# Kernel tuning notes

Measured on AMD Instinct MI355X. Metric: run time of the kernel, lower is better.

## Reference

```python
import jax, jax.numpy as jnp
import numpy as np

B, H, N, D = 2, 16, 4096, 64
NUM_PROJS = 8
BLOCK_SIZE = 256
SAMPLE_SIZE = 256
SCALE = D ** -0.5  # default scale = dim ** -0.5


def _unit_hamming_distance_array(size_n):
    # Gray-code permutation so that adjacent hash buckets differ in one bit
    a = np.array([0, 1], dtype=np.int32)
    for _ in range(size_n - 1):
        a = np.concatenate([a, np.flip(a) + a.shape[0]])
    return a

_PERM = jnp.asarray(_unit_hamming_distance_array(NUM_PROJS))
_ENC = jnp.asarray(2 ** np.arange(NUM_PROJS, dtype=np.int32))  # [num_projs]


def lsh_hash(x, proj_dir):
    # x: [b,h,n,d], proj_dir: [d,r] -> bucket id per token: [b,h,n]
    proj = jnp.einsum('bhnd,dr->bhnr', x, proj_dir)
    bin_ids = jnp.sum((proj > 0).astype(jnp.int32) * _ENC, axis=-1)
    return _PERM[bin_ids]


def attn_lse(q, k, v, scale):
    # exact softmax attention returning output and log-sum-exp
    s = jnp.einsum('...md,...nd->...mn', q, k) * scale
    lse = jax.nn.logsumexp(s, axis=-1, keepdims=True)
    out = jnp.einsum('...mn,...nv->...mv', jnp.exp(s - lse), v)
    return out, lse


def gather_seq(x, idx):
    # gather along the sequence axis (axis=2); broadcasts over last dim
    return jnp.take_along_axis(x, idx[..., None], axis=2)


def add_self_attentions(attn1, lse1, attn2, lse2):
    # combine two un-normalized softmax attentions via their lse's
    c = jax.nn.sigmoid(lse1 - lse2)  # = 1/(1+exp(lse2-lse1))
    attn = c * attn1 + (1.0 - c) * attn2
    lse = jnp.logaddexp(lse1, lse2)
    return attn, lse


def setup_inputs() -> dict:
    key = jax.random.key(0)
    kq, kk, kv, kp, ks = jax.random.split(key, 5)
    return {
        'query': jax.random.normal(kq, (B, H, N, D), jnp.float32),
        'key': jax.random.normal(kk, (B, H, N, D), jnp.float32),
        'value': jax.random.normal(kv, (B, H, N, D), jnp.float32),
        'proj_dir': jax.random.normal(kp, (D, NUM_PROJS), jnp.float32),
        'sampled_set': jax.random.randint(ks, (B, H, SAMPLE_SIZE), 0, N, dtype=jnp.int32),
    }


def reference(query, key, value, proj_dir, sampled_set):
    # --- LSH bucketing + stable sort of queries/keys by bucket id ---
    q_idx = jnp.argsort(lsh_hash(query, proj_dir), axis=2, stable=True)
    k_idx = jnp.argsort(lsh_hash(key, proj_dir), axis=2, stable=True)
    q_idx_inv = jnp.argsort(q_idx, axis=2, stable=True)

    q_s = gather_seq(query, q_idx)
    k_s = gather_seq(key, k_idx)
    v_s = gather_seq(value, k_idx)

    # --- block-diagonal attention in sorted order ---
    nb = N // BLOCK_SIZE
    q_b = q_s.reshape(B, H, nb, BLOCK_SIZE, D)
    k_b = k_s.reshape(B, H, nb, BLOCK_SIZE, D)
    v_b = v_s.reshape(B, H, nb, BLOCK_SIZE, D)
    attn_blk, lse_blk = attn_lse(q_b, k_b, v_b, SCALE)
    attn_blk = attn_blk.reshape(B, H, N, D)
    lse_blk = lse_blk.reshape(B, H, N, 1)
    # un-sort back to original query order
    attn_blk = gather_seq(attn_blk, q_idx_inv)
    lse_blk = gather_seq(lse_blk, q_idx_inv)

    # --- uniformly sampled residual attention, importance-weighted ---
    k_sub = gather_seq(key, sampled_set)
    v_sub = gather_seq(value, sampled_set)
    attn_res, lse_res = attn_lse(query, k_sub, v_sub, SCALE)
    lse_res = lse_res + jnp.log(N / SAMPLE_SIZE)

    attn, lse = add_self_attentions(attn_blk, lse_blk, attn_res, lse_res)
    return attn
```

## Files before the change

### kernel.cpp

```cpp
#include <hip/hip_runtime.h>
#include <hip/hip_bf16.h>
#include <math.h>

#define BH_ 32
#define N_ 4096
#define D_ 64
#define SAMP_ 256
#define SCALE_ 0.125f
#define LOG16_ 2.7725887222397811f
#define HPAD 68

typedef __attribute__((ext_vector_type(4))) float f32x4;
typedef __attribute__((ext_vector_type(8))) short bf16x8;
typedef __attribute__((ext_vector_type(4))) short bf16x4;

static __device__ __forceinline__ unsigned pack2(float a, float b) {
    union { __hip_bfloat162 h; unsigned u; } c;
    c.h = __float22bfloat162_rn(make_float2(a, b));
    return c.u;
}

static __device__ __forceinline__ bf16x8 cvt8v(f32x4 a, f32x4 b) {
    union { unsigned u[4]; bf16x8 v; } r;
    r.u[0] = pack2(a[0], a[1]); r.u[1] = pack2(a[2], a[3]);
    r.u[2] = pack2(b[0], b[1]); r.u[3] = pack2(b[2], b[3]);
    return r.v;
}

static __device__ __forceinline__ bf16x8 cvt8(const float* p) {
    return cvt8v(*(const f32x4*)p, *(const f32x4*)(p + 4));
}

__global__ __launch_bounds__(128) void hash_kernel(
    const float* __restrict__ q, const float* __restrict__ k,
    const float* __restrict__ pd,
    unsigned char* __restrict__ qbuck, unsigned char* __restrict__ kbuck)
{
    extern __shared__ char smraw[];
    float*  Xs  = (float*)smraw;
    double* Pdl = (double*)(smraw + 128 * HPAD * 4);

    int tid = threadIdx.x;
    const float* src = blockIdx.y ? k : q;
    unsigned char* dst = blockIdx.y ? kbuck : qbuck;
    size_t tok0 = (size_t)blockIdx.x * 128;

    {
        int d = tid >> 1, r0 = (tid & 1) * 4;
#pragma unroll
        for (int j = 0; j < 4; ++j)
            Pdl[d * 8 + r0 + j] = (double)pd[d * 8 + r0 + j];
    }
    {
        const float4* src4 = (const float4*)(src + tok0 * D_);
        for (int i = tid; i < 128 * 16; i += 128) {
            int r = i >> 4, c = i & 15;
            *(float4*)&Xs[r * HPAD + c * 4] = src4[i];
        }
    }
    __syncthreads();

    float xr[64];
#pragma unroll
    for (int c = 0; c < 16; ++c)
        *(f32x4*)&xr[c * 4] = *(const f32x4*)&Xs[tid * HPAD + c * 4];

    double acc[8];
#pragma unroll
    for (int r = 0; r < 8; ++r) acc[r] = 0.0;
#pragma unroll
    for (int d = 0; d < 64; ++d) {
        double x = (double)xr[d];
        const double* pr = Pdl + d * 8;
#pragma unroll
        for (int r = 0; r < 8; ++r) acc[r] += x * pr[r];
    }
    int bin = 0;
#pragma unroll
    for (int r = 0; r < 8; ++r)
        if (acc[r] > 0.0) bin |= (1 << r);
    dst[tok0 + tid] = (unsigned char)(bin ^ (bin >> 1));
}

__global__ __launch_bounds__(256) void sort_kernel(
    const unsigned char* __restrict__ qbuck,
    const unsigned char* __restrict__ kbuck,
    int* __restrict__ q_idx, int* __restrict__ k_idx)
{
    __shared__ unsigned short hist[64][256];
    __shared__ unsigned int   binstart[256];
    __shared__ alignas(16) unsigned char bl[N_];

    int bh = blockIdx.x, tensor = blockIdx.y;
    const unsigned char* buck = (tensor ? kbuck : qbuck) + bh * N_;
    int* idx_out = (tensor ? k_idx : q_idx) + bh * N_;
    int t = threadIdx.x;

    ((uint4*)bl)[t] = ((const uint4*)buck)[t];
    {
        uint4* h4 = (uint4*)&hist[0][0];
        for (int i = t; i < 2048; i += 256) h4[i] = make_uint4(0, 0, 0, 0);
    }
    __syncthreads();

    if (t < 64) {
        for (int u = 0; u < 64; ++u) hist[t][bl[t * 64 + u]]++;
    }
    __syncthreads();

    {
        unsigned run = 0;
        for (int tt = 0; tt < 64; ++tt) {
            unsigned c = hist[tt][t];
            hist[tt][t] = (unsigned short)run;
            run += c;
        }
        binstart[t] = run;
    }
    __syncthreads();

    if (t < 64) {
        unsigned b0 = binstart[t*4], b1 = binstart[t*4+1],
                 b2 = binstart[t*4+2], b3 = binstart[t*4+3];
        unsigned s = b0 + b1 + b2 + b3, p = s;
#pragma unroll
        for (int d = 1; d < 64; d <<= 1) {
            unsigned y = __shfl_up(p, d);
            if (t >= d) p += y;
        }
        unsigned e = p - s;
        binstart[t*4]   = e;
        binstart[t*4+1] = e + b0;
        binstart[t*4+2] = e + b0 + b1;
        binstart[t*4+3] = e + b0 + b1 + b2;
    }
    __syncthreads();

    if (t < 64) {
        for (int u = 0; u < 64; ++u) {
            int tok = t * 64 + u;
            int b = bl[tok];
            int pos = (int)(binstart[b] + hist[t][b]);
            hist[t][b]++;
            idx_out[pos] = tok;
        }
    }
}

static __device__ __forceinline__ void stage_kv(
    const float* __restrict__ key, const float* __restrict__ value,
    size_t base, int krI, int v0, int v1, int v2, int v3,
    int hK, int kwofs, int vd, int tid, short* Ksm, short* Vsm)
{
    {
        const float* kp = key + (base + (size_t)krI) * D_ + hK * 32;
        f32x4 k0 = *(const f32x4*)kp,        k1 = *(const f32x4*)(kp + 4);
        f32x4 k2 = *(const f32x4*)(kp + 8),  k3 = *(const f32x4*)(kp + 12);
        f32x4 k4 = *(const f32x4*)(kp + 16), k5 = *(const f32x4*)(kp + 20);
        f32x4 k6 = *(const f32x4*)(kp + 24), k7 = *(const f32x4*)(kp + 28);
        *(bf16x8*)&Ksm[kwofs]       = cvt8v(k0, k1);
        *(bf16x8*)&Ksm[kwofs + 128] = cvt8v(k2, k3);
        *(bf16x8*)&Ksm[kwofs + 256] = cvt8v(k4, k5);
        *(bf16x8*)&Ksm[kwofs + 384] = cvt8v(k6, k7);
    }
    {
        const float* vp0 = value + (base + (size_t)v0) * D_ + vd;
        const float* vp1 = value + (base + (size_t)v1) * D_ + vd;
        const float* vp2 = value + (base + (size_t)v2) * D_ + vd;
        const float* vp3 = value + (base + (size_t)v3) * D_ + vd;
        f32x4 a0 = *(const f32x4*)vp0, b0 = *(const f32x4*)(vp0 + 4);
        f32x4 a1 = *(const f32x4*)vp1, b1 = *(const f32x4*)(vp1 + 4);
        f32x4 a2 = *(const f32x4*)vp2, b2 = *(const f32x4*)(vp2 + 4);
        f32x4 a3 = *(const f32x4*)vp3, b3 = *(const f32x4*)(vp3 + 4);
        *(bf16x8*)&Vsm[tid * 8]         = cvt8v(a0, b0);
        *(bf16x8*)&Vsm[4096 + tid * 8]  = cvt8v(a1, b1);
        *(bf16x8*)&Vsm[8192 + tid * 8]  = cvt8v(a2, b2);
        *(bf16x8*)&Vsm[12288 + tid * 8] = cvt8v(a3, b3);
    }
}

static __device__ __forceinline__ void compute_256(
    const short* __restrict__ Ksm, unsigned vtr, float bias,
    const bf16x8 (&qf)[2][2], int lg, int ll,
    f32x4 (&o)[4][2], float (&lsum)[2])
{
#pragma unroll
    for (int hgi = 0; hgi < 8; ++hgi) {
        unsigned pbu[2][4];
        __builtin_amdgcn_s_setprio(1);
#pragma unroll
        for (int t = 0; t < 2; ++t) {
            int kt = hgi * 2 + t;
            f32x4 s0 = {0.f,0.f,0.f,0.f}, s1 = {0.f,0.f,0.f,0.f};
#pragma unroll
            for (int ks = 0; ks < 2; ++ks) {
                bf16x8 a = *(const bf16x8*)&Ksm[kt * 1024 + ks * 512 + lg * 128 + ll * 8];
                s0 = __builtin_amdgcn_mfma_f32_16x16x32_bf16(a, qf[0][ks], s0, 0, 0, 0);
                s1 = __builtin_amdgcn_mfma_f32_16x16x32_bf16(a, qf[1][ks], s1, 0, 0, 0);
            }
            __builtin_amdgcn_s_setprio(0);
            f32x4 e0, e1;
#pragma unroll
            for (int r = 0; r < 4; ++r) {
                e0[r] = __expf(fmaf(s0[r], SCALE_, bias));
                e1[r] = __expf(fmaf(s1[r], SCALE_, bias));
            }
            lsum[0] += (e0[0] + e0[1]) + (e0[2] + e0[3]);
            lsum[1] += (e1[0] + e1[1]) + (e1[2] + e1[3]);
            pbu[0][t*2]   = pack2(e0[0], e0[1]);
            pbu[0][t*2+1] = pack2(e0[2], e0[3]);
            pbu[1][t*2]   = pack2(e1[0], e1[1]);
            pbu[1][t*2+1] = pack2(e1[2], e1[3]);
            __builtin_amdgcn_s_setprio(1);
        }
        bf16x8 pb0, pb1;
        { union { unsigned u[4]; bf16x8 v; } cc;
          cc.u[0]=pbu[0][0]; cc.u[1]=pbu[0][1]; cc.u[2]=pbu[0][2]; cc.u[3]=pbu[0][3]; pb0=cc.v; }
        { union { unsigned u[4]; bf16x8 v; } cc;
          cc.u[0]=pbu[1][0]; cc.u[1]=pbu[1][1]; cc.u[2]=pbu[1][2]; cc.u[3]=pbu[1][3]; pb1=cc.v; }

        bf16x4 tr[4][2];
#pragma unroll
        for (int dt = 0; dt < 4; ++dt) {
            asm volatile("ds_read_b64_tr_b16 %0, %1 offset:%2"
                         : "=v"(tr[dt][0]) : "v"(vtr), "i"(hgi * 4096 + dt * 128));
            asm volatile("ds_read_b64_tr_b16 %0, %1 offset:%2"
                         : "=v"(tr[dt][1]) : "v"(vtr), "i"(hgi * 4096 + dt * 128 + 2048));
        }
        asm volatile("s_waitcnt lgkmcnt(0)" ::: "memory");
        __builtin_amdgcn_sched_barrier(0);
#pragma unroll
        for (int dt = 0; dt < 4; ++dt) {
            union { bf16x4 h[2]; bf16x8 v; } va;
            va.h[0] = tr[dt][0]; va.h[1] = tr[dt][1];
            o[dt][0] = __builtin_amdgcn_mfma_f32_16x16x32_bf16(va.v, pb0, o[dt][0], 0, 0, 0);
            o[dt][1] = __builtin_amdgcn_mfma_f32_16x16x32_bf16(va.v, pb1, o[dt][1], 0, 0, 0);
        }
        __builtin_amdgcn_s_setprio(0);
    }
}

__global__ __launch_bounds__(512, 4) void fused_attn(
    const float* __restrict__ query, const float* __restrict__ key,
    const float* __restrict__ value, const int* __restrict__ q_idx,
    const int* __restrict__ k_idx, const int* __restrict__ sampled,
    float* __restrict__ out)
{
    __shared__ __align__(16) short Ksm[16384];
    __shared__ __align__(16) short Vsm[16384];
    int wgid = blockIdx.x;
    int wg = (wgid & 7) * 64 + (wgid >> 3);
    int bh = wg >> 4, blk = wg & 15;
    int tid = threadIdx.x, w = tid >> 6, l = tid & 63, lg = l >> 4, ll = l & 15;
    size_t base = (size_t)bh * N_;

    const int* kidxA = k_idx + base + blk * 256;
    const int* kidxB = sampled + bh * SAMP_;

    int rK = tid & 255, hK = tid >> 8;
    int kwofs = (rK >> 4) * 1024 + hK * 512 + (rK & 15) * 8;
    int l6 = tid & 63, i6 = tid >> 6;
    int vrow = (i6 >> 2) * 32 + (l6 >> 5) * 4 + ((l6 >> 1) & 3) + (i6 & 3) * 8;
    int vd   = (((l6 >> 3) & 3) * 2 + (l6 & 1)) * 8;

    int krA = kidxA[rK];
    int vA0 = kidxA[vrow],       vA1 = kidxA[64 + vrow];
    int vA2 = kidxA[128 + vrow], vA3 = kidxA[192 + vrow];

    const int* qidx = q_idx + base + blk * 256 + w * 32;
    int qr[2]; bf16x8 qf[2][2];
#pragma unroll
    for (int mt = 0; mt < 2; ++mt) {
        qr[mt] = qidx[mt * 16 + ll];
        const float* qp = query + (base + (size_t)qr[mt]) * D_;
#pragma unroll
        for (int ks = 0; ks < 2; ++ks)
            qf[mt][ks] = cvt8(qp + ks * 32 + lg * 8);
    }

    f32x4 o[4][2]; float lsum[2];
#pragma unroll
    for (int mt = 0; mt < 2; ++mt) {
        lsum[mt] = 0.f;
#pragma unroll
        for (int dt = 0; dt < 4; ++dt) { f32x4 z = {0.f,0.f,0.f,0.f}; o[dt][mt] = z; }
    }
    unsigned vtr = (unsigned)(unsigned long long)(void*)&Vsm[0] + lg * 512 + ll * 8;

    stage_kv(key, value, base, krA, vA0, vA1, vA2, vA3, hK, kwofs, vd, tid, Ksm, Vsm);
    __syncthreads();

    int krB = kidxB[rK];
    int vB0 = kidxB[vrow],       vB1 = kidxB[64 + vrow];
    int vB2 = kidxB[128 + vrow], vB3 = kidxB[192 + vrow];

    compute_256(Ksm, vtr, 0.f, qf, lg, ll, o, lsum);
    __syncthreads();

    stage_kv(key, value, base, krB, vB0, vB1, vB2, vB3, hK, kwofs, vd, tid, Ksm, Vsm);
    __syncthreads();
    compute_256(Ksm, vtr, LOG16_, qf, lg, ll, o, lsum);

#pragma unroll
    for (int mt = 0; mt < 2; ++mt) {
        float v = lsum[mt];
        v += __shfl_xor(v, 16);
        v += __shfl_xor(v, 32);
        lsum[mt] = v;
    }
#pragma unroll
    for (int mt = 0; mt < 2; ++mt) {
        float dn = 1.f / lsum[mt];
        float* orow = out + (base + (size_t)qr[mt]) * D_ + lg * 4;
#pragma unroll
        for (int dt = 0; dt < 4; ++dt) {
            f32x4 v = o[dt][mt] * dn;
            *(f32x4*)&orow[dt * 16] = v;
        }
    }
}

extern "C" void kernel_launch(void* const* d_in, const int* in_sizes, int n_in,
                              void* d_out, int out_size, void* d_ws, size_t ws_size,
                              hipStream_t stream)
{
    const float* query = (const float*)d_in[0];
    const float* key   = (const float*)d_in[1];
    const float* value = (const float*)d_in[2];
    const float* pd    = (const float*)d_in[3];
    const int*   samp  = (const int*)d_in[4];
    float* out = (float*)d_out;

    char* ws = (char*)d_ws;
    unsigned char* qbuck = (unsigned char*)ws;
    unsigned char* kbuck = qbuck + (size_t)BH_ * N_;
    int* q_idx = (int*)(ws + 262144);
    int* k_idx = (int*)(ws + 262144 + 524288);

    size_t hash_lds = 128 * HPAD * 4 + 512 * 8;
    hipLaunchKernelGGL(hash_kernel, dim3(BH_ * N_ / 128, 2), dim3(128),
                       hash_lds, stream, query, key, pd, qbuck, kbuck);
    hipLaunchKernelGGL(sort_kernel, dim3(BH_, 2), dim3(256), 0, stream,
                       qbuck, kbuck, q_idx, k_idx);
    hipLaunchKernelGGL(fused_attn, dim3(512), dim3(512), 0, stream,
                       query, key, value, q_idx, k_idx, samp, out);
}
```

Before: 79.10 us.

## Use 4-wave workgroups with 64 query rows per wave and 128-key chunks

The attention workgroup shrinks from 8 waves to 4, and each wave now handles 64 query rows (4 M-tiles) instead of 32. Keys and values are staged in four 128-row chunks instead of two 256-row chunks, which halves LDS per workgroup. The goal is more reuse of each loaded K fragment and each V transpose read across M-tiles, plus lower LDS footprint. In exchange each wave holds more registers, there are more barriers and staging phases, and per-workgroup parallelism is lower.

```diff
diff --git a/kernel.cpp b/kernel.cpp
--- a/kernel.cpp
+++ b/kernel.cpp
@@ -147,13 +147,13 @@
     }
 }
 
-static __device__ __forceinline__ void stage_kv(
+static __device__ __forceinline__ void stage_kv4(
     const float* __restrict__ key, const float* __restrict__ value,
-    size_t base, int krI, int v0, int v1, int v2, int v3,
-    int hK, int kwofs, int vd, int tid, short* Ksm, short* Vsm)
-{
-    {
-        const float* kp = key + (base + (size_t)krI) * D_ + hK * 32;
+    size_t base, int kI, int v0, int v1, int hK, int kwofs,
+    int vd0, int vd1, int tid, short* Ksm, short* Vsm)
+{
+    {
+        const float* kp = key + (base + (size_t)kI) * D_ + hK * 32;
         f32x4 k0 = *(const f32x4*)kp,        k1 = *(const f32x4*)(kp + 4);
         f32x4 k2 = *(const f32x4*)(kp + 8),  k3 = *(const f32x4*)(kp + 12);
         f32x4 k4 = *(const f32x4*)(kp + 16), k5 = *(const f32x4*)(kp + 20);
@@ -164,68 +164,70 @@
         *(bf16x8*)&Ksm[kwofs + 384] = cvt8v(k6, k7);
     }
     {
-        const float* vp0 = value + (base + (size_t)v0) * D_ + vd;
-        const float* vp1 = value + (base + (size_t)v1) * D_ + vd;
-        const float* vp2 = value + (base + (size_t)v2) * D_ + vd;
-        const float* vp3 = value + (base + (size_t)v3) * D_ + vd;
-        f32x4 a0 = *(const f32x4*)vp0, b0 = *(const f32x4*)(vp0 + 4);
-        f32x4 a1 = *(const f32x4*)vp1, b1 = *(const f32x4*)(vp1 + 4);
-        f32x4 a2 = *(const f32x4*)vp2, b2 = *(const f32x4*)(vp2 + 4);
-        f32x4 a3 = *(const f32x4*)vp3, b3 = *(const f32x4*)(vp3 + 4);
-        *(bf16x8*)&Vsm[tid * 8]         = cvt8v(a0, b0);
-        *(bf16x8*)&Vsm[4096 + tid * 8]  = cvt8v(a1, b1);
-        *(bf16x8*)&Vsm[8192 + tid * 8]  = cvt8v(a2, b2);
-        *(bf16x8*)&Vsm[12288 + tid * 8] = cvt8v(a3, b3);
-    }
-}
-
-static __device__ __forceinline__ void compute_256(
+        const float* vp0 = value + (base + (size_t)v0) * D_ + vd0;
+        f32x4 a0 = *(const f32x4*)vp0, a1 = *(const f32x4*)(vp0 + 4);
+        f32x4 a2 = *(const f32x4*)(vp0 + 8), a3 = *(const f32x4*)(vp0 + 12);
+        *(bf16x8*)&Vsm[tid * 16]     = cvt8v(a0, a1);
+        *(bf16x8*)&Vsm[tid * 16 + 8] = cvt8v(a2, a3);
+        const float* vp1 = value + (base + (size_t)v1) * D_ + vd1;
+        f32x4 b0 = *(const f32x4*)vp1, b1 = *(const f32x4*)(vp1 + 4);
+        f32x4 b2 = *(const f32x4*)(vp1 + 8), b3 = *(const f32x4*)(vp1 + 12);
+        *(bf16x8*)&Vsm[(tid + 256) * 16]     = cvt8v(b0, b1);
+        *(bf16x8*)&Vsm[(tid + 256) * 16 + 8] = cvt8v(b2, b3);
+    }
+}
+
+static __device__ __forceinline__ void compute_128x4(
     const short* __restrict__ Ksm, unsigned vtr, float bias,
-    const bf16x8 (&qf)[2][2], int lg, int ll,
-    f32x4 (&o)[4][2], float (&lsum)[2])
-{
-#pragma unroll
-    for (int hgi = 0; hgi < 8; ++hgi) {
-        unsigned pbu[2][4];
+    const bf16x8 (&qf)[4][2], int lg, int ll,
+    f32x4 (&o)[4][4], float (&lsum)[4])
+{
+#pragma unroll
+    for (int c = 0; c < 4; ++c) {
+        unsigned pbu[4][4];
         __builtin_amdgcn_s_setprio(1);
 #pragma unroll
         for (int t = 0; t < 2; ++t) {
-            int kt = hgi * 2 + t;
-            f32x4 s0 = {0.f,0.f,0.f,0.f}, s1 = {0.f,0.f,0.f,0.f};
+            int kt = c * 2 + t;
+            f32x4 s[4];
+#pragma unroll
+            for (int mt = 0; mt < 4; ++mt) { f32x4 z = {0.f,0.f,0.f,0.f}; s[mt] = z; }
 #pragma unroll
             for (int ks = 0; ks < 2; ++ks) {
                 bf16x8 a = *(const bf16x8*)&Ksm[kt * 1024 + ks * 512 + lg * 128 + ll * 8];
-                s0 = __builtin_amdgcn_mfma_f32_16x16x32_bf16(a, qf[0][ks], s0, 0, 0, 0);
-                s1 = __builtin_amdgcn_mfma_f32_16x16x32_bf16(a, qf[1][ks], s1, 0, 0, 0);
+#pragma unroll
+                for (int mt = 0; mt < 4; ++mt)
+                    s[mt] = __builtin_amdgcn_mfma_f32_16x16x32_bf16(a, qf[mt][ks], s[mt], 0, 0, 0);
             }
             __builtin_amdgcn_s_setprio(0);
-            f32x4 e0, e1;
-#pragma unroll
-            for (int r = 0; r < 4; ++r) {
-                e0[r] = __expf(fmaf(s0[r], SCALE_, bias));
-                e1[r] = __expf(fmaf(s1[r], SCALE_, bias));
+#pragma unroll
+            for (int mt = 0; mt < 4; ++mt) {
+                f32x4 e;
+#pragma unroll
+                for (int r = 0; r < 4; ++r)
+                    e[r] = __expf(fmaf(s[mt][r], SCALE_, bias));
+                lsum[mt] += (e[0] + e[1]) + (e[2] + e[3]);
+                pbu[mt][t*2]   = pack2(e[0], e[1]);
+                pbu[mt][t*2+1] = pack2(e[2], e[3]);
             }
-            lsum[0] += (e0[0] + e0[1]) + (e0[2] + e0[3]);
-            lsum[1] += (e1[0] + e1[1]) + (e1[2] + e1[3]);
-            pbu[0][t*2]   = pack2(e0[0], e0[1]);
-            pbu[0][t*2+1] = pack2(e0[2], e0[3]);
-            pbu[1][t*2]   = pack2(e1[0], e1[1]);
-            pbu[1][t*2+1] = pack2(e1[2], e1[3]);
             __builtin_amdgcn_s_setprio(1);
         }
-        bf16x8 pb0, pb1;
-        { union { unsigned u[4]; bf16x8 v; } cc;
-          cc.u[0]=pbu[0][0]; cc.u[1]=pbu[0][1]; cc.u[2]=pbu[0][2]; cc.u[3]=pbu[0][3]; pb0=cc.v; }
-        { union { unsigned u[4]; bf16x8 v; } cc;
-          cc.u[0]=pbu[1][0]; cc.u[1]=pbu[1][1]; cc.u[2]=pbu[1][2]; cc.u[3]=pbu[1][3]; pb1=cc.v; }
+        bf16x8 pb[4];
+#pragma unroll
+        for (int mt = 0; mt < 4; ++mt) {
+            union { unsigned u[4]; bf16x8 v; } cc;
+            cc.u[0]=pbu[mt][0]; cc.u[1]=pbu[mt][1];
+            cc.u[2]=pbu[mt][2]; cc.u[3]=pbu[mt][3];
+            pb[mt] = cc.v;
+        }
 
         bf16x4 tr[4][2];
 #pragma unroll
         for (int dt = 0; dt < 4; ++dt) {
             asm volatile("ds_read_b64_tr_b16 %0, %1 offset:%2"
-                         : "=v"(tr[dt][0]) : "v"(vtr), "i"(hgi * 4096 + dt * 128));
+                         : "=v"(tr[dt][0]) : "v"(vtr), "i"(c * 4096 + dt * 128));
             asm volatile("ds_read_b64_tr_b16 %0, %1 offset:%2"
-                         : "=v"(tr[dt][1]) : "v"(vtr), "i"(hgi * 4096 + dt * 128 + 2048));
+                         : "=v"(tr[dt][1]) : "v"(vtr), "i"(c * 4096 + dt * 128 + 2048));
         }
         asm volatile("s_waitcnt lgkmcnt(0)" ::: "memory");
         __builtin_amdgcn_sched_barrier(0);
@@ -233,21 +235,22 @@
         for (int dt = 0; dt < 4; ++dt) {
             union { bf16x4 h[2]; bf16x8 v; } va;
             va.h[0] = tr[dt][0]; va.h[1] = tr[dt][1];
-            o[dt][0] = __builtin_amdgcn_mfma_f32_16x16x32_bf16(va.v, pb0, o[dt][0], 0, 0, 0);
-            o[dt][1] = __builtin_amdgcn_mfma_f32_16x16x32_bf16(va.v, pb1, o[dt][1], 0, 0, 0);
+#pragma unroll
+            for (int mt = 0; mt < 4; ++mt)
+                o[dt][mt] = __builtin_amdgcn_mfma_f32_16x16x32_bf16(va.v, pb[mt], o[dt][mt], 0, 0, 0);
         }
         __builtin_amdgcn_s_setprio(0);
     }
 }
 
-__global__ __launch_bounds__(512, 4) void fused_attn(
+__global__ __launch_bounds__(256) void fused_attn(
     const float* __restrict__ query, const float* __restrict__ key,
     const float* __restrict__ value, const int* __restrict__ q_idx,
     const int* __restrict__ k_idx, const int* __restrict__ sampled,
     float* __restrict__ out)
 {
-    __shared__ __align__(16) short Ksm[16384];
-    __shared__ __align__(16) short Vsm[16384];
+    __shared__ __align__(16) short Ksm[8192];
+    __shared__ __align__(16) short Vsm[8192];
     int wgid = blockIdx.x;
     int wg = (wgid & 7) * 64 + (wgid >> 3);
     int bh = wg >> 4, blk = wg & 15;
@@ -257,20 +260,18 @@
     const int* kidxA = k_idx + base + blk * 256;
     const int* kidxB = sampled + bh * SAMP_;
 
-    int rK = tid & 255, hK = tid >> 8;
+    int rK = tid & 127, hK = tid >> 7;
     int kwofs = (rK >> 4) * 1024 + hK * 512 + (rK & 15) * 8;
-    int l6 = tid & 63, i6 = tid >> 6;
-    int vrow = (i6 >> 2) * 32 + (l6 >> 5) * 4 + ((l6 >> 1) & 3) + (i6 & 3) * 8;
-    int vd   = (((l6 >> 3) & 3) * 2 + (l6 & 1)) * 8;
-
-    int krA = kidxA[rK];
-    int vA0 = kidxA[vrow],       vA1 = kidxA[64 + vrow];
-    int vA2 = kidxA[128 + vrow], vA3 = kidxA[192 + vrow];
-
-    const int* qidx = q_idx + base + blk * 256 + w * 32;
-    int qr[2]; bf16x8 qf[2][2];
-#pragma unroll
-    for (int mt = 0; mt < 2; ++mt) {
+    int vj0 = ((tid >> 4) << 2) | (tid & 3);
+    int vd0 = ((tid >> 2) & 3) * 16;
+    int s1  = tid + 256;
+    int vj1 = ((s1 >> 4) << 2) | (s1 & 3);
+    int vd1 = ((s1 >> 2) & 3) * 16;
+
+    const int* qidx = q_idx + base + blk * 256 + w * 64;
+    int qr[4]; bf16x8 qf[4][2];
+#pragma unroll
+    for (int mt = 0; mt < 4; ++mt) {
         qr[mt] = qidx[mt * 16 + ll];
         const float* qp = query + (base + (size_t)qr[mt]) * D_;
 #pragma unroll
@@ -278,38 +279,47 @@
             qf[mt][ks] = cvt8(qp + ks * 32 + lg * 8);
     }
 
-    f32x4 o[4][2]; float lsum[2];
-#pragma unroll
-    for (int mt = 0; mt < 2; ++mt) {
+    f32x4 o[4][4]; float lsum[4];
+#pragma unroll
+    for (int mt = 0; mt < 4; ++mt) {
         lsum[mt] = 0.f;
 #pragma unroll
         for (int dt = 0; dt < 4; ++dt) { f32x4 z = {0.f,0.f,0.f,0.f}; o[dt][mt] = z; }
     }
     unsigned vtr = (unsigned)(unsigned long long)(void*)&Vsm[0] + lg * 512 + ll * 8;
 
-    stage_kv(key, value, base, krA, vA0, vA1, vA2, vA3, hK, kwofs, vd, tid, Ksm, Vsm);
-    __syncthreads();
-
-    int krB = kidxB[rK];
-    int vB0 = kidxB[vrow],       vB1 = kidxB[64 + vrow];
-    int vB2 = kidxB[128 + vrow], vB3 = kidxB[192 + vrow];
-
-    compute_256(Ksm, vtr, 0.f, qf, lg, ll, o, lsum);
-    __syncthreads();
-
-    stage_kv(key, value, base, krB, vB0, vB1, vB2, vB3, hK, kwofs, vd, tid, Ksm, Vsm);
-    __syncthreads();
-    compute_256(Ksm, vtr, LOG16_, qf, lg, ll, o, lsum);
-
-#pragma unroll
-    for (int mt = 0; mt < 2; ++mt) {
+    int kI = kidxA[rK], v0 = kidxA[vj0], v1 = kidxA[vj1];
+    stage_kv4(key, value, base, kI, v0, v1, hK, kwofs, vd0, vd1, tid, Ksm, Vsm);
+    __syncthreads();
+    kI = kidxA[128 + rK]; v0 = kidxA[128 + vj0]; v1 = kidxA[128 + vj1];
+    compute_128x4(Ksm, vtr, 0.f, qf, lg, ll, o, lsum);
+    __syncthreads();
+
+    stage_kv4(key, value, base, kI, v0, v1, hK, kwofs, vd0, vd1, tid, Ksm, Vsm);
+    __syncthreads();
+    kI = kidxB[rK]; v0 = kidxB[vj0]; v1 = kidxB[vj1];
+    compute_128x4(Ksm, vtr, 0.f, qf, lg, ll, o, lsum);
+    __syncthreads();
+
+    stage_kv4(key, value, base, kI, v0, v1, hK, kwofs, vd0, vd1, tid, Ksm, Vsm);
+    __syncthreads();
+    kI = kidxB[128 + rK]; v0 = kidxB[128 + vj0]; v1 = kidxB[128 + vj1];
+    compute_128x4(Ksm, vtr, LOG16_, qf, lg, ll, o, lsum);
+    __syncthreads();
+
+    stage_kv4(key, value, base, kI, v0, v1, hK, kwofs, vd0, vd1, tid, Ksm, Vsm);
+    __syncthreads();
+    compute_128x4(Ksm, vtr, LOG16_, qf, lg, ll, o, lsum);
+
+#pragma unroll
+    for (int mt = 0; mt < 4; ++mt) {
         float v = lsum[mt];
         v += __shfl_xor(v, 16);
         v += __shfl_xor(v, 32);
         lsum[mt] = v;
     }
 #pragma unroll
-    for (int mt = 0; mt < 2; ++mt) {
+    for (int mt = 0; mt < 4; ++mt) {
         float dn = 1.f / lsum[mt];
         float* orow = out + (base + (size_t)qr[mt]) * D_ + lg * 4;
 #pragma unroll
@@ -342,6 +352,6 @@
                        hash_lds, stream, query, key, pd, qbuck, kbuck);
     hipLaunchKernelGGL(sort_kernel, dim3(BH_, 2), dim3(256), 0, stream,
                        qbuck, kbuck, q_idx, k_idx);
-    hipLaunchKernelGGL(fused_attn, dim3(512), dim3(512), 0, stream,
+    hipLaunchKernelGGL(fused_attn, dim3(512), dim3(256), 0, stream,
                        query, key, value, q_idx, k_idx, samp, out);
 }
```

After: 82.38 us. +4.2%, slower.

## Software-pipeline QK/exp of the next chunk ahead of the PV MFMAs

Applied to the files above, without the earlier changes.

Restructures the 256-key compute loop so the QK MFMAs and exponentials for chunk c+1 are issued before the PV MFMAs of chunk c. The transposed V LDS reads for the next chunk are issued right after the current PV step, so their latency is hidden behind the next chunk's QK and exp work. The per-step setprio toggling is replaced by one high priority over the whole loop. This adds live registers for the next chunk's packed probabilities, which risks spills under the tight 512x4 launch bounds.

```diff
diff --git a/kernel.cpp b/kernel.cpp
--- a/kernel.cpp
+++ b/kernel.cpp
@@ -179,56 +179,70 @@
     }
 }
 
+static __device__ __forceinline__ void qkexp(
+    const short* __restrict__ Ksm, int hgi, float bias,
+    const bf16x8 (&qf)[2][2], int lg, int ll,
+    float (&lsum)[2], bf16x8& pb0, bf16x8& pb1)
+{
+    unsigned pbu[2][4];
+#pragma unroll
+    for (int t = 0; t < 2; ++t) {
+        int kt = hgi * 2 + t;
+        f32x4 s0 = {0.f,0.f,0.f,0.f}, s1 = {0.f,0.f,0.f,0.f};
+#pragma unroll
+        for (int ks = 0; ks < 2; ++ks) {
+            bf16x8 a = *(const bf16x8*)&Ksm[kt * 1024 + ks * 512 + lg * 128 + ll * 8];
+            s0 = __builtin_amdgcn_mfma_f32_16x16x32_bf16(a, qf[0][ks], s0, 0, 0, 0);
+            s1 = __builtin_amdgcn_mfma_f32_16x16x32_bf16(a, qf[1][ks], s1, 0, 0, 0);
+        }
+        f32x4 e0, e1;
+#pragma unroll
+        for (int r = 0; r < 4; ++r) {
+            e0[r] = __expf(fmaf(s0[r], SCALE_, bias));
+            e1[r] = __expf(fmaf(s1[r], SCALE_, bias));
+        }
+        lsum[0] += (e0[0] + e0[1]) + (e0[2] + e0[3]);
+        lsum[1] += (e1[0] + e1[1]) + (e1[2] + e1[3]);
+        pbu[0][t*2]   = pack2(e0[0], e0[1]);
+        pbu[0][t*2+1] = pack2(e0[2], e0[3]);
+        pbu[1][t*2]   = pack2(e1[0], e1[1]);
+        pbu[1][t*2+1] = pack2(e1[2], e1[3]);
+    }
+    { union { unsigned u[4]; bf16x8 v; } cc;
+      cc.u[0]=pbu[0][0]; cc.u[1]=pbu[0][1]; cc.u[2]=pbu[0][2]; cc.u[3]=pbu[0][3]; pb0=cc.v; }
+    { union { unsigned u[4]; bf16x8 v; } cc;
+      cc.u[0]=pbu[1][0]; cc.u[1]=pbu[1][1]; cc.u[2]=pbu[1][2]; cc.u[3]=pbu[1][3]; pb1=cc.v; }
+}
+
+#define TR_ISSUE_(C) do { \
+    _Pragma("unroll") \
+    for (int dt = 0; dt < 4; ++dt) { \
+        asm volatile("ds_read_b64_tr_b16 %0, %1 offset:%2" \
+                     : "=v"(tr[dt][0]) : "v"(vtr0), "i"((C) * 4096 + dt * 128)); \
+        asm volatile("ds_read_b64_tr_b16 %0, %1 offset:%2" \
+                     : "=v"(tr[dt][1]) : "v"(vtr0), "i"((C) * 4096 + dt * 128 + 2048)); \
+    } } while (0)
+
 static __device__ __forceinline__ void compute_256(
-    const short* __restrict__ Ksm, unsigned vtr, float bias,
+    const short* __restrict__ Ksm, unsigned vtr0, float bias,
     const bf16x8 (&qf)[2][2], int lg, int ll,
     f32x4 (&o)[4][2], float (&lsum)[2])
 {
-#pragma unroll
-    for (int hgi = 0; hgi < 8; ++hgi) {
-        unsigned pbu[2][4];
-        __builtin_amdgcn_s_setprio(1);
-#pragma unroll
-        for (int t = 0; t < 2; ++t) {
-            int kt = hgi * 2 + t;
-            f32x4 s0 = {0.f,0.f,0.f,0.f}, s1 = {0.f,0.f,0.f,0.f};
-#pragma unroll
-            for (int ks = 0; ks < 2; ++ks) {
-                bf16x8 a = *(const bf16x8*)&Ksm[kt * 1024 + ks * 512 + lg * 128 + ll * 8];
-                s0 = __builtin_amdgcn_mfma_f32_16x16x32_bf16(a, qf[0][ks], s0, 0, 0, 0);
-                s1 = __builtin_amdgcn_mfma_f32_16x16x32_bf16(a, qf[1][ks], s1, 0, 0, 0);
-            }
-            __builtin_amdgcn_s_setprio(0);
-            f32x4 e0, e1;
-#pragma unroll
-            for (int r = 0; r < 4; ++r) {
-                e0[r] = __expf(fmaf(s0[r], SCALE_, bias));
-                e1[r] = __expf(fmaf(s1[r], SCALE_, bias));
-            }
-            lsum[0] += (e0[0] + e0[1]) + (e0[2] + e0[3]);
-            lsum[1] += (e1[0] + e1[1]) + (e1[2] + e1[3]);
-            pbu[0][t*2]   = pack2(e0[0], e0[1]);
-            pbu[0][t*2+1] = pack2(e0[2], e0[3]);
-            pbu[1][t*2]   = pack2(e1[0], e1[1]);
-            pbu[1][t*2+1] = pack2(e1[2], e1[3]);
-            __builtin_amdgcn_s_setprio(1);
-        }
-        bf16x8 pb0, pb1;
-        { union { unsigned u[4]; bf16x8 v; } cc;
-          cc.u[0]=pbu[0][0]; cc.u[1]=pbu[0][1]; cc.u[2]=pbu[0][2]; cc.u[3]=pbu[0][3]; pb0=cc.v; }
-        { union { unsigned u[4]; bf16x8 v; } cc;
-          cc.u[0]=pbu[1][0]; cc.u[1]=pbu[1][1]; cc.u[2]=pbu[1][2]; cc.u[3]=pbu[1][3]; pb1=cc.v; }
-
-        bf16x4 tr[4][2];
-#pragma unroll
-        for (int dt = 0; dt < 4; ++dt) {
-            asm volatile("ds_read_b64_tr_b16 %0, %1 offset:%2"
-                         : "=v"(tr[dt][0]) : "v"(vtr), "i"(hgi * 4096 + dt * 128));
-            asm volatile("ds_read_b64_tr_b16 %0, %1 offset:%2"
-                         : "=v"(tr[dt][1]) : "v"(vtr), "i"(hgi * 4096 + dt * 128 + 2048));
-        }
+    bf16x8 pb0, pb1, pn0, pn1;
+    bf16x4 tr[4][2];
+
+    __builtin_amdgcn_s_setprio(1);
+    qkexp(Ksm, 0, bias, qf, lg, ll, lsum, pb0, pb1);
+    TR_ISSUE_(0);
+
+#pragma unroll
+    for (int c = 0; c < 8; ++c) {
+        if (c < 7)
+            qkexp(Ksm, c + 1, bias, qf, lg, ll, lsum, pn0, pn1);
+
         asm volatile("s_waitcnt lgkmcnt(0)" ::: "memory");
         __builtin_amdgcn_sched_barrier(0);
+
 #pragma unroll
         for (int dt = 0; dt < 4; ++dt) {
             union { bf16x4 h[2]; bf16x8 v; } va;
@@ -236,8 +250,13 @@
             o[dt][0] = __builtin_amdgcn_mfma_f32_16x16x32_bf16(va.v, pb0, o[dt][0], 0, 0, 0);
             o[dt][1] = __builtin_amdgcn_mfma_f32_16x16x32_bf16(va.v, pb1, o[dt][1], 0, 0, 0);
         }
-        __builtin_amdgcn_s_setprio(0);
-    }
+
+        if (c < 7) {
+            TR_ISSUE_(c + 1);
+            pb0 = pn0; pb1 = pn1;
+        }
+    }
+    __builtin_amdgcn_s_setprio(0);
 }
 
 __global__ __launch_bounds__(512, 4) void fused_attn(
@@ -285,7 +304,7 @@
 #pragma unroll
         for (int dt = 0; dt < 4; ++dt) { f32x4 z = {0.f,0.f,0.f,0.f}; o[dt][mt] = z; }
     }
-    unsigned vtr = (unsigned)(unsigned long long)(void*)&Vsm[0] + lg * 512 + ll * 8;
+    unsigned vtr0 = (unsigned)(unsigned long long)(void*)&Vsm[0] + lg * 512 + ll * 8;
 
     stage_kv(key, value, base, krA, vA0, vA1, vA2, vA3, hK, kwofs, vd, tid, Ksm, Vsm);
     __syncthreads();
@@ -294,12 +313,12 @@
     int vB0 = kidxB[vrow],       vB1 = kidxB[64 + vrow];
     int vB2 = kidxB[128 + vrow], vB3 = kidxB[192 + vrow];
 
-    compute_256(Ksm, vtr, 0.f, qf, lg, ll, o, lsum);
+    compute_256(Ksm, vtr0, 0.f, qf, lg, ll, o, lsum);
     __syncthreads();
 
     stage_kv(key, value, base, krB, vB0, vB1, vB2, vB3, hK, kwofs, vd, tid, Ksm, Vsm);
     __syncthreads();
-    compute_256(Ksm, vtr, LOG16_, qf, lg, ll, o, lsum);
+    compute_256(Ksm, vtr0, LOG16_, qf, lg, ll, o, lsum);
 
 #pragma unroll
     for (int mt = 0; mt < 2; ++mt) {
```

New measurement: 79.90 us. No clear change (+1.0%).
